# Kernel optimization log

Hardware: AMD Instinct MI355X
Metric: run time of the kernel (lower is better)

Reference implementation:

```python
import jax, jax.numpy as jnp
import numpy as np

N_NODES = 100000
N_EDGES = 50000
NNZ = 800000
D_IN = 128
D_OUT = 128


def setup_inputs() -> dict:
    key = jax.random.key(0)
    k1, k2, k3, k4, k5 = jax.random.split(key, 5)
    x_0 = jax.random.normal(k1, (N_NODES, D_IN), dtype=jnp.float32)
    W = jax.random.normal(k2, (D_OUT, D_IN), dtype=jnp.float32) / np.sqrt(D_IN)
    b = jax.random.normal(k3, (D_OUT,), dtype=jnp.float32) * 0.01
    node_ids = jax.random.randint(k4, (NNZ,), 0, N_NODES, dtype=jnp.int32)
    edge_ids = jax.random.randint(k5, (NNZ,), 0, N_EDGES, dtype=jnp.int32)
    return {"x_0": x_0, "W": W, "b": b, "node_ids": node_ids, "edge_ids": edge_ids}


def reference(x_0, W, b, node_ids, edge_ids):
    # Linear transform (no batchnorm: use_bn=False)
    x = x_0 @ W.T + b  # [n_nodes, out_channels]

    # Step 1: hyperedge aggregation (e_aggr='sum'):  m_{0->1} = B_1^T x, reduce=sum
    m01 = jax.ops.segment_sum(x[node_ids], edge_ids, num_segments=N_EDGES)  # [n_edges, d]

    # Step 2: node aggregation (v_aggr='mean'):  m_{1->0} = B_1 m_{0->1}, reduce=mean
    s = jax.ops.segment_sum(m01[edge_ids], node_ids, num_segments=N_NODES)  # [n_nodes, d]
    cnt = jax.ops.segment_sum(jnp.ones((NNZ,), dtype=x.dtype), node_ids, num_segments=N_NODES)
    m10 = s / jnp.maximum(cnt, 1.0)[:, None]

    # Step 3: SAGE update (residual add)
    return x + m10
```

## Files before the change

### kernel.cpp

```cpp
#include <hip/hip_runtime.h>
#include <hip/hip_bf16.h>

#define NN 100000
#define NE 50000
#define NZ 800000
#define D  128
#define NSEG (NE + NN)
#define FILL_P 4
#define FILL_B 782

typedef __bf16 bf16x8 __attribute__((ext_vector_type(8)));
typedef float f32x4 __attribute__((ext_vector_type(4)));

static __device__ __forceinline__ unsigned short f2bf(float f) {
  union { float f; unsigned u; } v; v.f = f;
  unsigned r = (v.u + 0x7FFFu + ((v.u >> 16) & 1u)) >> 16;
  return (unsigned short)r;
}
static __device__ __forceinline__ float bf2f(unsigned short h) {
  union { unsigned u; float f; } v; v.u = ((unsigned)h) << 16;
  return v.f;
}

__global__ __launch_bounds__(256) void unisage_gemm_mfma(const float* __restrict__ x0,
                                                         const float* __restrict__ W,
                                                         const float* __restrict__ bias,
                                                         unsigned short* __restrict__ xb) {
  __shared__ __bf16 Wl[128][136];
  const int t = threadIdx.x;
#pragma unroll
  for (int i = 0; i < 16; ++i) {
    int idx = i * 1024 + t * 4;
    int dout = idx >> 7;
    int k = idx & 127;
    float4 wv = *(const float4*)(W + idx);
    Wl[dout][k + 0] = (__bf16)wv.x;
    Wl[dout][k + 1] = (__bf16)wv.y;
    Wl[dout][k + 2] = (__bf16)wv.z;
    Wl[dout][k + 3] = (__bf16)wv.w;
  }
  __syncthreads();

  const int wave = t >> 6;
  const int lane = t & 63;
  const int lr = lane & 15;
  const int lg = lane >> 4;
  const int rowbase = blockIdx.x * 128 + wave * 32;

  f32x4 acc[2][8] = {};

#pragma unroll
  for (int ks = 0; ks < 4; ++ks) {
    const int k0 = ks * 32 + lg * 8;
    bf16x8 wf[8];
#pragma unroll
    for (int cf = 0; cf < 8; ++cf)
      wf[cf] = *(const bf16x8*)&Wl[cf * 16 + lr][k0];
#pragma unroll
    for (int rf = 0; rf < 2; ++rf) {
      int row = rowbase + rf * 16 + lr;
      row = row < NN ? row : NN - 1;
      const float* src = x0 + (size_t)row * D + k0;
      float4 f0 = *(const float4*)(src);
      float4 f1 = *(const float4*)(src + 4);
      bf16x8 xf;
      xf[0] = (__bf16)f0.x; xf[1] = (__bf16)f0.y;
      xf[2] = (__bf16)f0.z; xf[3] = (__bf16)f0.w;
      xf[4] = (__bf16)f1.x; xf[5] = (__bf16)f1.y;
      xf[6] = (__bf16)f1.z; xf[7] = (__bf16)f1.w;
#pragma unroll
      for (int cf = 0; cf < 8; ++cf)
        acc[rf][cf] = __builtin_amdgcn_mfma_f32_16x16x32_bf16(wf[cf], xf, acc[rf][cf], 0, 0, 0);
    }
  }

#pragma unroll
  for (int cf = 0; cf < 8; ++cf) {
    float4 bv = *(const float4*)(bias + cf * 16 + lg * 4);
#pragma unroll
    for (int rf = 0; rf < 2; ++rf) {
      int row = rowbase + rf * 16 + lr;
      if (row < NN) {
        ushort4 o;
        o.x = f2bf(acc[rf][cf][0] + bv.x);
        o.y = f2bf(acc[rf][cf][1] + bv.y);
        o.z = f2bf(acc[rf][cf][2] + bv.z);
        o.w = f2bf(acc[rf][cf][3] + bv.w);
        *(ushort4*)(xb + (size_t)row * D + cf * 16 + lg * 4) = o;
      }
    }
  }
}

__global__ void unisage_hist_rank(const int* __restrict__ nid, const int* __restrict__ eid,
                                  int* __restrict__ cnt,
                                  unsigned short* __restrict__ rank_e,
                                  unsigned short* __restrict__ rank_n) {
  int i = blockIdx.x * 256 + threadIdx.x;
  if (i >= NZ) return;
  int e = eid[i], v = nid[i];
  rank_e[i] = (unsigned short)atomicAdd(&cnt[e], 1);
  rank_n[i] = (unsigned short)atomicAdd(&cnt[NE + v], 1);
}

__global__ void unisage_scan_k1(const int* __restrict__ in, int* __restrict__ bsum, int n) {
  __shared__ int sh[256];
  int t = threadIdx.x;
  int base = blockIdx.x * 1024 + t * 4;
  int s = 0;
#pragma unroll
  for (int j = 0; j < 4; ++j)
    if (base + j < n) s += in[base + j];
  sh[t] = s;
  __syncthreads();
  for (int o = 128; o > 0; o >>= 1) {
    if (t < o) sh[t] += sh[t + o];
    __syncthreads();
  }
  if (t == 0) bsum[blockIdx.x] = sh[0];
}

__global__ void unisage_scan_k3(const int* __restrict__ in, const int* __restrict__ bsum,
                                int* __restrict__ out, int n, int nb) {
  __shared__ int sh[256];
  int t = threadIdx.x;
  int bv = (t < nb) ? bsum[t] : 0;
  sh[t] = bv;
  __syncthreads();
  for (int o = 1; o < 256; o <<= 1) {
    int add = (t >= o) ? sh[t - o] : 0;
    __syncthreads();
    sh[t] += add;
    __syncthreads();
  }
  int bbase = (blockIdx.x == 0) ? 0 : sh[blockIdx.x - 1];
  __syncthreads();

  int base = blockIdx.x * 1024 + t * 4;
  int v[4];
#pragma unroll
  for (int j = 0; j < 4; ++j) v[j] = (base + j < n) ? in[base + j] : 0;
  int tsum = v[0] + v[1] + v[2] + v[3];
  sh[t] = tsum;
  __syncthreads();
  for (int o = 1; o < 256; o <<= 1) {
    int add = (t >= o) ? sh[t - o] : 0;
    __syncthreads();
    sh[t] += add;
    __syncthreads();
  }
  int run = sh[t] - tsum + bbase;
#pragma unroll
  for (int j = 0; j < 4; ++j) {
    if (base + j < n) out[base + j] = run;
    run += v[j];
  }
}

__global__ void unisage_fill(const int* __restrict__ nid, const int* __restrict__ eid,
                             const unsigned short* __restrict__ rank_e,
                             const unsigned short* __restrict__ rank_n,
                             const int* __restrict__ off,
                             int* __restrict__ csr_e, int* __restrict__ csr_n) {
  const int R = (NSEG + FILL_P - 1) / FILL_P;
  int pass = blockIdx.x / FILL_B;
  int base = ((blockIdx.x % FILL_B) * 256 + threadIdx.x) * 4;
  if (base >= NZ) return;
  int lo = pass * R, hi = lo + R;
  int4 e4 = *(const int4*)(eid + base);
  int4 n4 = *(const int4*)(nid + base);
  ushort4 re4 = *(const ushort4*)(rank_e + base);
  ushort4 rn4 = *(const ushort4*)(rank_n + base);
  int e[4] = {e4.x, e4.y, e4.z, e4.w};
  int v[4] = {n4.x, n4.y, n4.z, n4.w};
  unsigned short re[4] = {re4.x, re4.y, re4.z, re4.w};
  unsigned short rn[4] = {rn4.x, rn4.y, rn4.z, rn4.w};
#pragma unroll
  for (int j = 0; j < 4; ++j) {
    if (e[j] >= lo && e[j] < hi) csr_e[off[e[j]] + (int)re[j]] = v[j];
    int s = NE + v[j];
    if (s >= lo && s < hi) csr_n[off[s] + (int)rn[j] - NZ] = e[j];
  }
}

#define QRED(x) { x += __shfl_xor(x, 16, 64); x += __shfl_xor(x, 32, 64); }

__global__ void unisage_edge_agg(const unsigned short* __restrict__ xb,
                                 const int* __restrict__ csr_e,
                                 const int* __restrict__ off, const int* __restrict__ cnt,
                                 unsigned short* __restrict__ m01b) {
  int w = (blockIdx.x * 256 + threadIdx.x) >> 6;
  int lane = threadIdx.x & 63;
  if (w >= NE) return;
  int quad = lane >> 4;
  int sl = lane & 15;
  int beg = off[w];
  int deg = cnt[w];
  int end = beg + deg;
  float a0 = 0, a1 = 0, a2 = 0, a3 = 0, a4 = 0, a5 = 0, a6 = 0, a7 = 0;
  for (int base = beg; base < end; base += 64) {
    int m = min(64, end - base);
    int idx = (lane < m) ? csr_e[base + lane] : 0;
    int iters = (m + 3) >> 2;
    for (int jj = 0; jj < iters; ++jj) {
      int p = 4 * jj + quad;
      int r = __shfl(idx, p, 64);
      if (p < m) {
        uint4 vv = *(const uint4*)(xb + (size_t)r * D + sl * 8);
        a0 += bf2f((unsigned short)(vv.x & 0xffffu)); a1 += bf2f((unsigned short)(vv.x >> 16));
        a2 += bf2f((unsigned short)(vv.y & 0xffffu)); a3 += bf2f((unsigned short)(vv.y >> 16));
        a4 += bf2f((unsigned short)(vv.z & 0xffffu)); a5 += bf2f((unsigned short)(vv.z >> 16));
        a6 += bf2f((unsigned short)(vv.w & 0xffffu)); a7 += bf2f((unsigned short)(vv.w >> 16));
      }
    }
  }
  QRED(a0) QRED(a1) QRED(a2) QRED(a3) QRED(a4) QRED(a5) QRED(a6) QRED(a7)
  if (quad == 0) {
    uint4 o;
    o.x = (unsigned)f2bf(a0) | ((unsigned)f2bf(a1) << 16);
    o.y = (unsigned)f2bf(a2) | ((unsigned)f2bf(a3) << 16);
    o.z = (unsigned)f2bf(a4) | ((unsigned)f2bf(a5) << 16);
    o.w = (unsigned)f2bf(a6) | ((unsigned)f2bf(a7) << 16);
    *(uint4*)(m01b + (size_t)w * D + sl * 8) = o;
  }
}

__global__ void unisage_node_agg(const unsigned short* __restrict__ xb,
                                 const unsigned short* __restrict__ m01b,
                                 const int* __restrict__ csr_n,
                                 const int* __restrict__ off, const int* __restrict__ cnt,
                                 float* __restrict__ out) {
  int wv = (blockIdx.x * 256 + threadIdx.x) >> 6;
  int lane = threadIdx.x & 63;
  int half = lane >> 5;
  int sub = lane & 31;
  int rg = sub >> 4;
  int sl = sub & 15;
  int w = wv * 2 + half;
  if (w >= NN) return;
  int deg = cnt[NE + w];
  int beg = off[NE + w] - NZ;
  int end = beg + deg;
  float a0 = 0, a1 = 0, a2 = 0, a3 = 0, a4 = 0, a5 = 0, a6 = 0, a7 = 0;
  for (int base = beg; base < end; base += 32) {
    int m = min(32, end - base);
    int idx = (sub < m) ? csr_n[base + sub] : 0;
    int iters = (m + 1) >> 1;
    for (int jj = 0; jj < iters; ++jj) {
      int p = 2 * jj + rg;
      int r = __shfl(idx, half * 32 + p, 64);
      if (p < m) {
        uint4 vv = *(const uint4*)(m01b + (size_t)r * D + sl * 8);
        a0 += bf2f((unsigned short)(vv.x & 0xffffu)); a1 += bf2f((unsigned short)(vv.x >> 16));
        a2 += bf2f((unsigned short)(vv.y & 0xffffu)); a3 += bf2f((unsigned short)(vv.y >> 16));
        a4 += bf2f((unsigned short)(vv.z & 0xffffu)); a5 += bf2f((unsigned short)(vv.z >> 16));
        a6 += bf2f((unsigned short)(vv.w & 0xffffu)); a7 += bf2f((unsigned short)(vv.w >> 16));
      }
    }
  }
  a0 += __shfl_xor(a0, 16, 64); a1 += __shfl_xor(a1, 16, 64);
  a2 += __shfl_xor(a2, 16, 64); a3 += __shfl_xor(a3, 16, 64);
  a4 += __shfl_xor(a4, 16, 64); a5 += __shfl_xor(a5, 16, 64);
  a6 += __shfl_xor(a6, 16, 64); a7 += __shfl_xor(a7, 16, 64);
  if (rg == 0) {
    float inv = 1.0f / fmaxf((float)deg, 1.0f);
    uint4 xr = *(const uint4*)(xb + (size_t)w * D + sl * 8);
    f32x4 o0, o1;
    o0[0] = bf2f((unsigned short)(xr.x & 0xffffu)) + a0 * inv;
    o0[1] = bf2f((unsigned short)(xr.x >> 16))     + a1 * inv;
    o0[2] = bf2f((unsigned short)(xr.y & 0xffffu)) + a2 * inv;
    o0[3] = bf2f((unsigned short)(xr.y >> 16))     + a3 * inv;
    o1[0] = bf2f((unsigned short)(xr.z & 0xffffu)) + a4 * inv;
    o1[1] = bf2f((unsigned short)(xr.z >> 16))     + a5 * inv;
    o1[2] = bf2f((unsigned short)(xr.w & 0xffffu)) + a6 * inv;
    o1[3] = bf2f((unsigned short)(xr.w >> 16))     + a7 * inv;
    __builtin_nontemporal_store(o0, (f32x4*)(out + (size_t)w * D + sl * 8));
    __builtin_nontemporal_store(o1, (f32x4*)(out + (size_t)w * D + sl * 8 + 4));
  }
}

extern "C" void kernel_launch(void* const* d_in, const int* in_sizes, int n_in,
                              void* d_out, int out_size, void* d_ws, size_t ws_size,
                              hipStream_t stream) {
  const float* x0   = (const float*)d_in[0];
  const float* W    = (const float*)d_in[1];
  const float* bias = (const float*)d_in[2];
  const int* nid    = (const int*)d_in[3];
  const int* eid    = (const int*)d_in[4];
  float* out = (float*)d_out;

  unsigned short* xb   = (unsigned short*)d_ws;
  unsigned short* m01b = xb + (size_t)NN * D;
  int* cnt   = (int*)(m01b + (size_t)NE * D);
  int* off   = cnt + 150016;
  unsigned short* rank_e = (unsigned short*)(off + 150016);
  unsigned short* rank_n = rank_e + NZ;
  int* csr_e = (int*)(rank_n + NZ);
  int* csr_n = csr_e + NZ;
  int* bsum  = csr_n + NZ;

  hipMemsetAsync(cnt, 0, NSEG * sizeof(int), stream);

  unisage_hist_rank<<<NZ / 256, 256, 0, stream>>>(nid, eid, cnt, rank_e, rank_n);

  unisage_gemm_mfma<<<(NN + 127) / 128, 256, 0, stream>>>(x0, W, bias, xb);

  const int nb = (NSEG + 1023) / 1024;
  unisage_scan_k1<<<nb, 256, 0, stream>>>(cnt, bsum, NSEG);
  unisage_scan_k3<<<nb, 256, 0, stream>>>(cnt, bsum, off, NSEG, nb);

  unisage_fill<<<FILL_P * FILL_B, 256, 0, stream>>>(nid, eid, rank_e, rank_n, off, csr_e, csr_n);

  unisage_edge_agg<<<(NE * 64) / 256, 256, 0, stream>>>(xb, csr_e, off, cnt, m01b);
  unisage_node_agg<<<(NN / 2 * 64) / 256, 256, 0, stream>>>(xb, m01b, csr_n, off, cnt, out);
}
```

Measured before the change: 206.1 us.

## Fuse histogram/rank pass into GEMM kernel via block-role split

```diff
diff --git a/kernel.cpp b/kernel.cpp
--- a/kernel.cpp
+++ b/kernel.cpp
@@ -8,6 +8,8 @@
 #define NSEG (NE + NN)
 #define FILL_P 4
 #define FILL_B 782
+#define G_GEMM 782
+#define G_HIST 391
 
 typedef __bf16 bf16x8 __attribute__((ext_vector_type(8)));
 typedef float f32x4 __attribute__((ext_vector_type(4)));
@@ -22,85 +24,103 @@
   return v.f;
 }
 
-__global__ __launch_bounds__(256) void unisage_gemm_mfma(const float* __restrict__ x0,
+__global__ __launch_bounds__(256) void unisage_gemm_hist(const float* __restrict__ x0,
                                                          const float* __restrict__ W,
                                                          const float* __restrict__ bias,
-                                                         unsigned short* __restrict__ xb) {
+                                                         unsigned short* __restrict__ xb,
+                                                         const int* __restrict__ nid,
+                                                         const int* __restrict__ eid,
+                                                         int* __restrict__ cnt,
+                                                         unsigned short* __restrict__ rank_e,
+                                                         unsigned short* __restrict__ rank_n) {
   __shared__ __bf16 Wl[128][136];
-  const int t = threadIdx.x;
-#pragma unroll
-  for (int i = 0; i < 16; ++i) {
-    int idx = i * 1024 + t * 4;
-    int dout = idx >> 7;
-    int k = idx & 127;
-    float4 wv = *(const float4*)(W + idx);
-    Wl[dout][k + 0] = (__bf16)wv.x;
-    Wl[dout][k + 1] = (__bf16)wv.y;
-    Wl[dout][k + 2] = (__bf16)wv.z;
-    Wl[dout][k + 3] = (__bf16)wv.w;
-  }
-  __syncthreads();
-
-  const int wave = t >> 6;
-  const int lane = t & 63;
-  const int lr = lane & 15;
-  const int lg = lane >> 4;
-  const int rowbase = blockIdx.x * 128 + wave * 32;
-
-  f32x4 acc[2][8] = {};
-
-#pragma unroll
-  for (int ks = 0; ks < 4; ++ks) {
-    const int k0 = ks * 32 + lg * 8;
-    bf16x8 wf[8];
-#pragma unroll
-    for (int cf = 0; cf < 8; ++cf)
-      wf[cf] = *(const bf16x8*)&Wl[cf * 16 + lr][k0];
-#pragma unroll
-    for (int rf = 0; rf < 2; ++rf) {
-      int row = rowbase + rf * 16 + lr;
-      row = row < NN ? row : NN - 1;
-      const float* src = x0 + (size_t)row * D + k0;
-      float4 f0 = *(const float4*)(src);
-      float4 f1 = *(const float4*)(src + 4);
-      bf16x8 xf;
-      xf[0] = (__bf16)f0.x; xf[1] = (__bf16)f0.y;
-      xf[2] = (__bf16)f0.z; xf[3] = (__bf16)f0.w;
-      xf[4] = (__bf16)f1.x; xf[5] = (__bf16)f1.y;
-      xf[6] = (__bf16)f1.z; xf[7] = (__bf16)f1.w;
+  if (blockIdx.x < G_GEMM) {
+    const int t = threadIdx.x;
+#pragma unroll
+    for (int i = 0; i < 16; ++i) {
+      int idx = i * 1024 + t * 4;
+      int dout = idx >> 7;
+      int k = idx & 127;
+      float4 wv = *(const float4*)(W + idx);
+      Wl[dout][k + 0] = (__bf16)wv.x;
+      Wl[dout][k + 1] = (__bf16)wv.y;
+      Wl[dout][k + 2] = (__bf16)wv.z;
+      Wl[dout][k + 3] = (__bf16)wv.w;
+    }
+    __syncthreads();
+
+    const int wave = t >> 6;
+    const int lane = t & 63;
+    const int lr = lane & 15;
+    const int lg = lane >> 4;
+    const int rowbase = blockIdx.x * 128 + wave * 32;
+
+    f32x4 acc[2][8] = {};
+
+#pragma unroll
+    for (int ks = 0; ks < 4; ++ks) {
+      const int k0 = ks * 32 + lg * 8;
+      bf16x8 wf[8];
 #pragma unroll
       for (int cf = 0; cf < 8; ++cf)
-        acc[rf][cf] = __builtin_amdgcn_mfma_f32_16x16x32_bf16(wf[cf], xf, acc[rf][cf], 0, 0, 0);
-    }
-  }
-
-#pragma unroll
-  for (int cf = 0; cf < 8; ++cf) {
-    float4 bv = *(const float4*)(bias + cf * 16 + lg * 4);
-#pragma unroll
-    for (int rf = 0; rf < 2; ++rf) {
-      int row = rowbase + rf * 16 + lr;
-      if (row < NN) {
-        ushort4 o;
-        o.x = f2bf(acc[rf][cf][0] + bv.x);
-        o.y = f2bf(acc[rf][cf][1] + bv.y);
-        o.z = f2bf(acc[rf][cf][2] + bv.z);
-        o.w = f2bf(acc[rf][cf][3] + bv.w);
-        *(ushort4*)(xb + (size_t)row * D + cf * 16 + lg * 4) = o;
+        wf[cf] = *(const bf16x8*)&Wl[cf * 16 + lr][k0];
+#pragma unroll
+      for (int rf = 0; rf < 2; ++rf) {
+        int row = rowbase + rf * 16 + lr;
+        row = row < NN ? row : NN - 1;
+        const float* src = x0 + (size_t)row * D + k0;
+        float4 f0 = *(const float4*)(src);
+        float4 f1 = *(const float4*)(src + 4);
+        bf16x8 xf;
+        xf[0] = (__bf16)f0.x; xf[1] = (__bf16)f0.y;
+        xf[2] = (__bf16)f0.z; xf[3] = (__bf16)f0.w;
+        xf[4] = (__bf16)f1.x; xf[5] = (__bf16)f1.y;
+        xf[6] = (__bf16)f1.z; xf[7] = (__bf16)f1.w;
+#pragma unroll
+        for (int cf = 0; cf < 8; ++cf)
+          acc[rf][cf] = __builtin_amdgcn_mfma_f32_16x16x32_bf16(wf[cf], xf, acc[rf][cf], 0, 0, 0);
       }
     }
-  }
-}
-
-__global__ void unisage_hist_rank(const int* __restrict__ nid, const int* __restrict__ eid,
-                                  int* __restrict__ cnt,
-                                  unsigned short* __restrict__ rank_e,
-                                  unsigned short* __restrict__ rank_n) {
-  int i = blockIdx.x * 256 + threadIdx.x;
-  if (i >= NZ) return;
-  int e = eid[i], v = nid[i];
-  rank_e[i] = (unsigned short)atomicAdd(&cnt[e], 1);
-  rank_n[i] = (unsigned short)atomicAdd(&cnt[NE + v], 1);
+
+#pragma unroll
+    for (int cf = 0; cf < 8; ++cf) {
+      float4 bv = *(const float4*)(bias + cf * 16 + lg * 4);
+#pragma unroll
+      for (int rf = 0; rf < 2; ++rf) {
+        int row = rowbase + rf * 16 + lr;
+        if (row < NN) {
+          ushort4 o;
+          o.x = f2bf(acc[rf][cf][0] + bv.x);
+          o.y = f2bf(acc[rf][cf][1] + bv.y);
+          o.z = f2bf(acc[rf][cf][2] + bv.z);
+          o.w = f2bf(acc[rf][cf][3] + bv.w);
+          *(ushort4*)(xb + (size_t)row * D + cf * 16 + lg * 4) = o;
+        }
+      }
+    }
+  } else {
+    int base = ((blockIdx.x - G_GEMM) * 256 + threadIdx.x) * 8;
+    if (base >= NZ) return;
+    int4 ea = *(const int4*)(eid + base);
+    int4 eb = *(const int4*)(eid + base + 4);
+    int4 na = *(const int4*)(nid + base);
+    int4 nb = *(const int4*)(nid + base + 4);
+    int e[8] = {ea.x, ea.y, ea.z, ea.w, eb.x, eb.y, eb.z, eb.w};
+    int v[8] = {na.x, na.y, na.z, na.w, nb.x, nb.y, nb.z, nb.w};
+    unsigned short re[8], rn[8];
+#pragma unroll
+    for (int j = 0; j < 8; ++j) re[j] = (unsigned short)atomicAdd(&cnt[e[j]], 1);
+#pragma unroll
+    for (int j = 0; j < 8; ++j) rn[j] = (unsigned short)atomicAdd(&cnt[NE + v[j]], 1);
+    ushort4 r0 = {re[0], re[1], re[2], re[3]};
+    ushort4 r1 = {re[4], re[5], re[6], re[7]};
+    ushort4 s0 = {rn[0], rn[1], rn[2], rn[3]};
+    ushort4 s1 = {rn[4], rn[5], rn[6], rn[7]};
+    *(ushort4*)(rank_e + base) = r0;
+    *(ushort4*)(rank_e + base + 4) = r1;
+    *(ushort4*)(rank_n + base) = s0;
+    *(ushort4*)(rank_n + base + 4) = s1;
+  }
 }
 
 __global__ void unisage_scan_k1(const int* __restrict__ in, int* __restrict__ bsum, int n) {
@@ -301,9 +321,8 @@
 
   hipMemsetAsync(cnt, 0, NSEG * sizeof(int), stream);
 
-  unisage_hist_rank<<<NZ / 256, 256, 0, stream>>>(nid, eid, cnt, rank_e, rank_n);
-
-  unisage_gemm_mfma<<<(NN + 127) / 128, 256, 0, stream>>>(x0, W, bias, xb);
+  unisage_gemm_hist<<<G_GEMM + G_HIST, 256, 0, stream>>>(x0, W, bias, xb, nid, eid,
+                                                         cnt, rank_e, rank_n);
 
   const int nb = (NSEG + 1023) / 1024;
   unisage_scan_k1<<<nb, 256, 0, stream>>>(cnt, bsum, NSEG);
```

New measurement: 199.3 us. 3.3% less time.
